# Kernel tuning notes

Hardware: AMD Instinct MI355X
Metric: run time of the kernel (lower is better)

Reference implementation:

```python
import jax, jax.numpy as jnp
import numpy as np

F = 128   # num_features
H = 128   # hidden sizes
U = 128   # u_size == out_size
N = 50000
E = 600000
B = 64
L = 4     # hops + 1 layers


def _scatter_mean(vals, idx, num_segments):
    s = jax.ops.segment_sum(vals, idx, num_segments=num_segments)
    cnt = jax.ops.segment_sum(jnp.ones((vals.shape[0],), vals.dtype), idx,
                              num_segments=num_segments)
    return s / jnp.maximum(cnt, 1.0)[:, None]


def setup_inputs() -> dict:
    key = jax.random.key(0)
    ks = jax.random.split(key, 20)
    x = jax.random.normal(ks[0], (N, F), jnp.float32)
    edge_index = jax.random.randint(ks[1], (2, E), 0, N, jnp.int64)
    u = jax.random.normal(ks[2], (B, U), jnp.float32)
    batch = jnp.sort(jax.random.randint(ks[3], (N,), 0, B, jnp.int64))
    sc = 0.05
    # stacked per-layer params (all layer dims identical since u_size==out_size)
    params = {
        'n1w1': jax.random.normal(ks[4], (L, F, H), jnp.float32) * sc,
        'n1b1': jnp.zeros((L, H), jnp.float32),
        'n1w2': jax.random.normal(ks[5], (L, H, H), jnp.float32) * sc,
        'n1b2': jnp.zeros((L, H), jnp.float32),
        'n2w1': jax.random.normal(ks[6], (L, F + H + U, H), jnp.float32) * sc,
        'n2b1': jnp.zeros((L, H), jnp.float32),
        'n2w2': jax.random.normal(ks[7], (L, H, F), jnp.float32) * sc,
        'n2b2': jnp.zeros((L, F), jnp.float32),
        'gw1': jax.random.normal(ks[8], (L, F + U, H), jnp.float32) * sc,
        'gb1': jnp.zeros((L, H), jnp.float32),
        'gw2': jax.random.normal(ks[9], (L, H, U), jnp.float32) * sc,
        'gb2': jnp.zeros((L, U), jnp.float32),
    }
    return dict(x=x, edge_index=edge_index, u=u, batch=batch, **params)


def reference(x, edge_index, u, batch,
              n1w1, n1b1, n1w2, n1b2, n2w1, n2b1, n2w2, n2b2,
              gw1, gb1, gw2, gb2):
    row, col = edge_index[0], edge_index[1]
    for l in range(L):
        # NodeModel
        m = jax.nn.relu(x[row] @ n1w1[l] + n1b1[l]) @ n1w2[l] + n1b2[l]  # [E,H]
        agg = _scatter_mean(m, col, N)                                    # [N,H]
        h = jnp.concatenate([x, agg, u[batch]], axis=1)                   # [N,F+H+U]
        x = jax.nn.relu(h @ n2w1[l] + n2b1[l]) @ n2w2[l] + n2b2[l]        # [N,F]
        # GlobalModel (uses updated x)
        g = jnp.concatenate([u, _scatter_mean(x, batch, B)], axis=1)      # [B,F+U]
        u = jax.nn.relu(g @ gw1[l] + gb1[l]) @ gw2[l] + gb2[l]            # [B,U]
    return (x, u)
```

## Files before the change

kernel.cpp:

```cpp
#include <hip/hip_runtime.h>

typedef __bf16 bf16;
typedef bf16 bf16x8 __attribute__((ext_vector_type(8)));
typedef bf16 bf16x4 __attribute__((ext_vector_type(4)));
typedef bf16 bf16x2 __attribute__((ext_vector_type(2)));
typedef float floatx4 __attribute__((ext_vector_type(4)));

#define MFMA __builtin_amdgcn_mfma_f32_16x16x32_bf16

__device__ __forceinline__ float bfhi_f(unsigned u) {
  const unsigned x = u << 16;
  return __builtin_bit_cast(float, x);
}
__device__ __forceinline__ float bflo_f(unsigned u) {
  const unsigned x = u & 0xffff0000u;
  return __builtin_bit_cast(float, x);
}

__device__ __forceinline__ void bar_lds() {
  asm volatile("s_waitcnt lgkmcnt(0)" ::: "memory");
  __builtin_amdgcn_s_barrier();
}


__global__ void hist_kernel(const int* __restrict__ ei, int* __restrict__ cnt, int E) {
  int e = blockIdx.x * blockDim.x + threadIdx.x;
  if (e < E) atomicAdd(&cnt[ei[E + e]], 1);
}

__global__ void gcnt_kernel(const int* __restrict__ batch, int* __restrict__ gcnt,
                            int N, int B) {
  const int b = threadIdx.x;
  if (b >= B) return;
  auto lb = [&](int v) {
    int lo = 0, hi = N;
    while (lo < hi) {
      const int mid = (lo + hi) >> 1;
      if (batch[mid] < v) lo = mid + 1; else hi = mid;
    }
    return lo;
  };
  gcnt[b] = lb(b + 1) - lb(b);
}

__global__ void scan1_kernel(const int* __restrict__ cnt, int* __restrict__ colptr,
                             int* __restrict__ rctr, int* __restrict__ btot, int n) {
  __shared__ int sd[256];
  const int tid = threadIdx.x;
  const int i0 = blockIdx.x * 2048 + tid * 8;
  int v[8];
  int tot = 0;
#pragma unroll
  for (int j = 0; j < 8; ++j) {
    const int i = i0 + j;
    v[j] = (i < n) ? cnt[i] : 0;
    tot += v[j];
  }
  sd[tid] = tot;
  __syncthreads();
  for (int off = 1; off < 256; off <<= 1) {
    const int t = (tid >= off) ? sd[tid - off] : 0;
    __syncthreads();
    sd[tid] += t;
    __syncthreads();
  }
  int excl = sd[tid] - tot;
#pragma unroll
  for (int j = 0; j < 8; ++j) {
    const int i = i0 + j;
    if (i < n) { colptr[i] = excl; rctr[i] = excl; }
    excl += v[j];
  }
  if (tid == 255) btot[blockIdx.x] = sd[255];
}

__global__ void scan2_kernel(int* __restrict__ colptr, int* __restrict__ rctr,
                             const int* __restrict__ btot, int n) {
  __shared__ int off_s;
  const int tid = threadIdx.x;
  if (blockIdx.x == 0) return;
  if (tid == 0) {
    int o = 0;
    for (int j = 0; j < (int)blockIdx.x; ++j) o += btot[j];
    off_s = o;
  }
  __syncthreads();
  const int off = off_s;
  const int i0 = blockIdx.x * 2048 + tid * 8;
#pragma unroll
  for (int j = 0; j < 8; ++j) {
    const int i = i0 + j;
    if (i < n) { colptr[i] += off; rctr[i] += off; }
  }
}

__global__ void place_kernel(const int* __restrict__ ei, int* __restrict__ rctr,
                             int* __restrict__ esrow, int E) {
  int e = blockIdx.x * blockDim.x + threadIdx.x;
  if (e >= E) return;
  const int r = ei[e];
  const int c = ei[E + e];
  const int p = atomicAdd(&rctr[c], 1);
  esrow[p] = r;
}

__global__ void wsplit_kernel(const float* __restrict__ src, bf16* __restrict__ dst,
                              int Ksrc, int K, int HH) {
  const int l = blockIdx.y;
  const int gid = blockIdx.x * blockDim.x + threadIdx.x;
  if (gid >= K * HH) return;
  const int h = gid / K, k = gid - h * K;
  const float v = src[(size_t)l * Ksrc * HH + (size_t)k * HH + h];
  const bf16 hi = (bf16)v;
  const bf16 lo = (bf16)(v - (float)hi);
  bf16* d = dst + (size_t)l * 2 * K * HH;
  d[(size_t)h * K + k] = hi;
  d[(size_t)K * HH + (size_t)h * K + k] = lo;
}

__global__ void wfuse_kernel(const float* __restrict__ n2w1,
                             const float* __restrict__ n1w2,
                             float* __restrict__ G) {
  const int l = blockIdx.y, k = blockIdx.x, h = threadIdx.x;
  const float* w = n2w1 + (size_t)l * 384 * 128;
  float* g = G + (size_t)l * 256 * 128;
  g[(size_t)k * 128 + h] = w[(size_t)k * 128 + h];
  const float* a = n1w2 + (size_t)l * 128 * 128 + (size_t)k * 128;
  float s = 0.f;
#pragma unroll 8
  for (int j = 0; j < 128; ++j)
    s = fmaf(a[j], w[(size_t)(128 + j) * 128 + h], s);
  g[(size_t)(128 + k) * 128 + h] = s;
}

__global__ void xsplit_kernel(const float* __restrict__ x, bf16* __restrict__ xhi,
                              bf16* __restrict__ xlo, int n4) {
  const int i = blockIdx.x * 256 + threadIdx.x;
  if (i >= n4) return;
  const float4 v = ((const float4*)x)[i];
  bf16x4 h, l;
  const float vv[4] = {v.x, v.y, v.z, v.w};
#pragma unroll
  for (int r = 0; r < 4; ++r) {
    h[r] = (bf16)vv[r];
    l[r] = (bf16)(vv[r] - (float)h[r]);
  }
  *(bf16x4*)&xhi[(size_t)i * 4] = h;
  *(bf16x4*)&xlo[(size_t)i * 4] = l;
}

__global__ __launch_bounds__(256, 3)
void pnode_mfma(const bf16* __restrict__ xh, const bf16* __restrict__ xl,
                const bf16* __restrict__ w1t, const float* __restrict__ b1,
                bf16* __restrict__ P, int N) {
  __shared__ __align__(16) bf16 R[64 * 136];

  const int tid = threadIdx.x;
  const int n0 = blockIdx.x * 64;
  const int wave = tid >> 6, lane = tid & 63, q = lane >> 4, lr = lane & 15;
  const int hbase = wave * 32;

  int nn[4];
#pragma unroll
  for (int nt = 0; nt < 4; ++nt) {
    int n = n0 + nt * 16 + lr;
    nn[nt] = (n > N - 1) ? (N - 1) : n;
  }

  const floatx4 zz = {0.f, 0.f, 0.f, 0.f};
  floatx4 acc[2][4];
#pragma unroll
  for (int mt = 0; mt < 2; ++mt)
#pragma unroll
    for (int nt = 0; nt < 4; ++nt) acc[mt][nt] = zz;

  {
    bf16x8 bh[2][4], bl[2][4], ah[2][2], al[2][2];
    auto loadA = [&](int kc, int buf) {
#pragma unroll
      for (int mt = 0; mt < 2; ++mt) {
        const bf16* wp = w1t + (size_t)(hbase + mt * 16 + lr) * 128 + kc * 32 + q * 8;
        ah[buf][mt] = *(const bf16x8*)wp;
        al[buf][mt] = *(const bf16x8*)(wp + 16384);
      }
    };
    auto loadB = [&](int kc, int buf) {
#pragma unroll
      for (int nt = 0; nt < 4; ++nt) {
        const size_t off = (size_t)nn[nt] * 128 + kc * 32 + q * 8;
        bh[buf][nt] = *(const bf16x8*)(xh + off);
        bl[buf][nt] = *(const bf16x8*)(xl + off);
      }
    };
    loadA(0, 0);
    loadB(0, 0);
#pragma unroll
    for (int kc = 0; kc < 4; ++kc) {
      const int cur = kc & 1, nxt = cur ^ 1;
      if (kc < 3) {
        loadA(kc + 1, nxt);
        loadB(kc + 1, nxt);
      }
#pragma unroll
      for (int nt = 0; nt < 4; ++nt)
#pragma unroll
        for (int mt = 0; mt < 2; ++mt) {
          acc[mt][nt] = MFMA(ah[cur][mt], bh[cur][nt], acc[mt][nt], 0, 0, 0);
          acc[mt][nt] = MFMA(al[cur][mt], bh[cur][nt], acc[mt][nt], 0, 0, 0);
          acc[mt][nt] = MFMA(ah[cur][mt], bl[cur][nt], acc[mt][nt], 0, 0, 0);
        }
    }
  }

#pragma unroll
  for (int mt = 0; mt < 2; ++mt) {
    const int h0 = hbase + mt * 16 + q * 4;
    const float* bp = &b1[h0];
#pragma unroll
    for (int nt = 0; nt < 4; ++nt) {
      const int e = nt * 16 + lr;
      bf16x4 hh;
#pragma unroll
      for (int r = 0; r < 4; ++r)
        hh[r] = (bf16)fmaxf(acc[mt][nt][r] + bp[r], 0.f);
      *(bf16x4*)&R[e * 136 + h0] = hh;
    }
  }
  bar_lds();
#pragma unroll
  for (int it = 0; it < 4; ++it) {
    const int idx = it * 256 + tid;
    const int row = idx >> 4;
    const int f8 = (idx & 15) * 8;
    const int n = n0 + row;
    if (n < N)
      *(bf16x8*)&P[(size_t)n * 128 + f8] = *(const bf16x8*)&R[row * 136 + f8];
  }
}

__global__ __launch_bounds__(256, 8)
void agg_csr(const bf16* __restrict__ P, const int* __restrict__ colptr,
             const int* __restrict__ esrow,
             bf16* __restrict__ aggh, bf16* __restrict__ aggl, int N, int E) {
  const int lane = threadIdx.x & 63;
  const int c = blockIdx.x * 4 + (threadIdx.x >> 6);
  if (c >= N) return;
  const int beg = colptr[c];
  const int end = (c == N - 1) ? E : colptr[c + 1];
  float s0[4] = {0.f, 0.f, 0.f, 0.f};
  float s1[4] = {0.f, 0.f, 0.f, 0.f};
  int e = beg;
  for (; e + 8 <= end; e += 8) {
    int r[8];
#pragma unroll
    for (int j = 0; j < 8; ++j) r[j] = esrow[e + j];
    unsigned v[8];
#pragma unroll
    for (int j = 0; j < 8; ++j)
      v[j] = *(const unsigned*)&P[(size_t)r[j] * 128 + lane * 2];
#pragma unroll
    for (int j = 0; j < 8; ++j) {
      s0[j & 3] += bfhi_f(v[j]);
      s1[j & 3] += bflo_f(v[j]);
    }
  }
  const int rem = end - e;
  if (rem > 0) {
    int r[8];
#pragma unroll
    for (int j = 0; j < 8; ++j) r[j] = esrow[e + (j < rem ? j : 0)];
    unsigned v[8];
#pragma unroll
    for (int j = 0; j < 8; ++j)
      v[j] = *(const unsigned*)&P[(size_t)r[j] * 128 + lane * 2];
#pragma unroll
    for (int j = 0; j < 8; ++j) {
      if (j < rem) {
        s0[j & 3] += bfhi_f(v[j]);
        s1[j & 3] += bflo_f(v[j]);
      }
    }
  }
  const int cc = end - beg;
  const float inv = 1.f / (float)(cc > 1 ? cc : 1);
  const float v0 = ((s0[0] + s0[1]) + (s0[2] + s0[3])) * inv;
  const float v1 = ((s1[0] + s1[1]) + (s1[2] + s1[3])) * inv;
  bf16x2 h, l;
  h[0] = (bf16)v0;  l[0] = (bf16)(v0 - (float)h[0]);
  h[1] = (bf16)v1;  l[1] = (bf16)(v1 - (float)h[1]);
  *(bf16x2*)&aggh[(size_t)c * 128 + lane * 2] = h;
  *(bf16x2*)&aggl[(size_t)c * 128 + lane * 2] = l;
}

__global__ __launch_bounds__(256, 3)
void node_p(bf16* xh, bf16* xl,
            const bf16* __restrict__ aggh, const bf16* __restrict__ aggl,
            const float* __restrict__ UW, const int* __restrict__ batch,
            const bf16* __restrict__ w1t, const bf16* __restrict__ w2t,
            const float* __restrict__ b2,
            const bf16* __restrict__ w1te, const float* __restrict__ b1e,
            bf16* __restrict__ Pout, float* __restrict__ gx,
            float* __restrict__ xout, int write_x, int has_next, int N) {
  __shared__ __align__(16) bf16 R[2 * 64 * 136];
  __shared__ int sbatch[64];

  const int tid = threadIdx.x;
  const int n0 = blockIdx.x * 64;
  const int wave = tid >> 6, lane = tid & 63, q = lane >> 4, lr = lane & 15;
  const int hbase = wave * 32;

  if (tid < 64) {
    int n = n0 + tid;
    sbatch[tid] = batch[(n > N - 1) ? (N - 1) : n];
  }

  int nn[4], ub[4];
#pragma unroll
  for (int nt = 0; nt < 4; ++nt) {
    int n = n0 + nt * 16 + lr;
    if (n > N - 1) n = N - 1;
    nn[nt] = n;
    ub[nt] = batch[n];
  }

  floatx4 acc[2][4];
#pragma unroll
  for (int mt = 0; mt < 2; ++mt)
#pragma unroll
    for (int nt = 0; nt < 4; ++nt)
      acc[mt][nt] = *(const floatx4*)&UW[(size_t)ub[nt] * 128 + hbase + mt * 16 + q * 4];

  {
    bf16x8 bh[2][4], bl[2][4], ah[2][2], al[2][2];
    auto loadB = [&](int kc, int buf) {
#pragma unroll
      for (int nt = 0; nt < 4; ++nt) {
        if (kc < 4) {
          const size_t off = (size_t)nn[nt] * 128 + kc * 32 + q * 8;
          bh[buf][nt] = *(const bf16x8*)(xh + off);
          bl[buf][nt] = *(const bf16x8*)(xl + off);
        } else {
          const size_t off = (size_t)nn[nt] * 128 + (kc - 4) * 32 + q * 8;
          bh[buf][nt] = *(const bf16x8*)(aggh + off);
          bl[buf][nt] = *(const bf16x8*)(aggl + off);
        }
      }
    };
    auto loadA = [&](int kc, int buf) {
#pragma unroll
      for (int mt = 0; mt < 2; ++mt) {
        const bf16* wp = w1t + (size_t)(hbase + mt * 16 + lr) * 256 + kc * 32 + q * 8;
        ah[buf][mt] = *(const bf16x8*)wp;
        al[buf][mt] = *(const bf16x8*)(wp + 32768);
      }
    };
    loadA(0, 0);
    loadB(0, 0);
#pragma unroll
    for (int kc = 0; kc < 8; ++kc) {
      const int cur = kc & 1, nxt = cur ^ 1;
      if (kc < 7) {
        loadA(kc + 1, nxt);
        loadB(kc + 1, nxt);
      }
#pragma unroll
      for (int nt = 0; nt < 4; ++nt)
#pragma unroll
        for (int mt = 0; mt < 2; ++mt) {
          acc[mt][nt] = MFMA(ah[cur][mt], bh[cur][nt], acc[mt][nt], 0, 0, 0);
          acc[mt][nt] = MFMA(al[cur][mt], bh[cur][nt], acc[mt][nt], 0, 0, 0);
          acc[mt][nt] = MFMA(ah[cur][mt], bl[cur][nt], acc[mt][nt], 0, 0, 0);
        }
    }
  }

  bf16x8 a2h[2][2], a2l[2][2];
#pragma unroll
  for (int mt = 0; mt < 2; ++mt) {
    const bf16* wp = w2t + (size_t)(hbase + mt * 16 + lr) * 128 + q * 8;
    a2h[0][mt] = *(const bf16x8*)wp;
    a2l[0][mt] = *(const bf16x8*)(wp + 16384);
  }

  const floatx4 zz = {0.f, 0.f, 0.f, 0.f};
#pragma unroll
  for (int mt = 0; mt < 2; ++mt) {
    const int h0 = hbase + mt * 16 + q * 4;
#pragma unroll
    for (int nt = 0; nt < 4; ++nt) {
      const int e = nt * 16 + lr;
      bf16x4 hh, ll;
#pragma unroll
      for (int r = 0; r < 4; ++r) {
        const float v = fmaxf(acc[mt][nt][r], 0.f);
        hh[r] = (bf16)v;
        ll[r] = (bf16)(v - (float)hh[r]);
      }
      *(bf16x4*)&R[e * 136 + h0] = hh;
      *(bf16x4*)&R[64 * 136 + e * 136 + h0] = ll;
      acc[mt][nt] = zz;
    }
  }
  bar_lds();

#pragma unroll
  for (int ks = 0; ks < 4; ++ks) {
    const int cur = ks & 1, nxt = cur ^ 1;
    if (ks < 3) {
#pragma unroll
      for (int mt = 0; mt < 2; ++mt) {
        const bf16* wp = w2t + (size_t)(hbase + mt * 16 + lr) * 128 + (ks + 1) * 32 + q * 8;
        a2h[nxt][mt] = *(const bf16x8*)wp;
        a2l[nxt][mt] = *(const bf16x8*)(wp + 16384);
      }
    }
    bf16x8 b2h[4], b2l[4];
#pragma unroll
    for (int nt = 0; nt < 4; ++nt) {
      const bf16* hp = &R[(nt * 16 + lr) * 136 + ks * 32 + q * 8];
      b2h[nt] = *(const bf16x8*)hp;
      b2l[nt] = *(const bf16x8*)(hp + 64 * 136);
    }
#pragma unroll
    for (int nt = 0; nt < 4; ++nt)
#pragma unroll
      for (int mt = 0; mt < 2; ++mt) {
        acc[mt][nt] = MFMA(a2h[cur][mt], b2h[nt], acc[mt][nt], 0, 0, 0);
        acc[mt][nt] = MFMA(a2l[cur][mt], b2h[nt], acc[mt][nt], 0, 0, 0);
        acc[mt][nt] = MFMA(a2h[cur][mt], b2l[nt], acc[mt][nt], 0, 0, 0);
      }
  }
  bar_lds();

  bf16x8 pah[2][2], pal[2][2];
  if (has_next) {
#pragma unroll
    for (int mt = 0; mt < 2; ++mt) {
      const bf16* wp = w1te + (size_t)(hbase + mt * 16 + lr) * 128 + q * 8;
      pah[0][mt] = *(const bf16x8*)wp;
      pal[0][mt] = *(const bf16x8*)(wp + 16384);
    }
  }

  float* Xt = (float*)&R[0];
#pragma unroll
  for (int mt = 0; mt < 2; ++mt) {
    const int f0 = hbase + mt * 16 + q * 4;
    const float* bp = &b2[f0];
#pragma unroll
    for (int nt = 0; nt < 4; ++nt) {
      const int e = nt * 16 + lr;
      const int n = n0 + e;
      float4 o;
      o.x = (n < N) ? acc[mt][nt][0] + bp[0] : 0.f;
      o.y = (n < N) ? acc[mt][nt][1] + bp[1] : 0.f;
      o.z = (n < N) ? acc[mt][nt][2] + bp[2] : 0.f;
      o.w = (n < N) ? acc[mt][nt][3] + bp[3] : 0.f;
      *(float4*)&Xt[e * 132 + f0] = o;
    }
  }
  bar_lds();

  if (has_next) {
#pragma unroll
    for (int it = 0; it < 4; ++it) {
      const int idx = it * 256 + tid;
      const int row = idx >> 4;
      const int f8 = (idx & 15) * 8;
      const int n = n0 + row;
      if (n < N) {
        bf16x8 hh, ll;
#pragma unroll
        for (int j = 0; j < 8; ++j) {
          const float v = Xt[row * 132 + f8 + j];
          hh[j] = (bf16)v;
          ll[j] = (bf16)(v - (float)hh[j]);
        }
        *(bf16x8*)&xh[(size_t)n * 128 + f8] = hh;
        *(bf16x8*)&xl[(size_t)n * 128 + f8] = ll;
      }
    }
  }
  if (write_x) {
#pragma unroll
    for (int it = 0; it < 8; ++it) {
      const int idx = it * 256 + tid;
      const int row = idx >> 5;
      const int f4 = (idx & 31) * 4;
      const int n = n0 + row;
      if (n < N)
        *(float4*)&xout[(size_t)n * 128 + f4] = *(const float4*)&Xt[row * 132 + f4];
    }
  }

  {
    const int f = tid & 127;
    const int es = (tid >> 7) * 32;
    int cur = sbatch[es];
    float s = 0.f;
    for (int e = es; e < es + 32; ++e) {
      const int b = sbatch[e];
      const float v = Xt[e * 132 + f];
      if (b != cur) {
        atomicAdd(&gx[(size_t)cur * 128 + f], s);
        s = 0.f;
        cur = b;
      }
      s += v;
    }
    atomicAdd(&gx[(size_t)cur * 128 + f], s);
  }

  if (!has_next) return;

  floatx4 pacc[2][4];
#pragma unroll
  for (int mt = 0; mt < 2; ++mt)
#pragma unroll
    for (int nt = 0; nt < 4; ++nt) pacc[mt][nt] = zz;

#pragma unroll
  for (int kc = 0; kc < 4; ++kc) {
    const int cur = kc & 1, nxt = cur ^ 1;
    if (kc < 3) {
#pragma unroll
      for (int mt = 0; mt < 2; ++mt) {
        const bf16* wp = w1te + (size_t)(hbase + mt * 16 + lr) * 128 + (kc + 1) * 32 + q * 8;
        pah[nxt][mt] = *(const bf16x8*)wp;
        pal[nxt][mt] = *(const bf16x8*)(wp + 16384);
      }
    }
    bf16x8 bh[4], bl[4];
#pragma unroll
    for (int nt = 0; nt < 4; ++nt) {
      const float* xp = &Xt[(nt * 16 + lr) * 132 + kc * 32 + q * 8];
#pragma unroll
      for (int r = 0; r < 8; ++r) {
        const float v = xp[r];
        bh[nt][r] = (bf16)v;
        bl[nt][r] = (bf16)(v - (float)bh[nt][r]);
      }
    }
#pragma unroll
    for (int nt = 0; nt < 4; ++nt)
#pragma unroll
      for (int mt = 0; mt < 2; ++mt) {
        pacc[mt][nt] = MFMA(pah[cur][mt], bh[nt], pacc[mt][nt], 0, 0, 0);
        pacc[mt][nt] = MFMA(pal[cur][mt], bh[nt], pacc[mt][nt], 0, 0, 0);
        pacc[mt][nt] = MFMA(pah[cur][mt], bl[nt], pacc[mt][nt], 0, 0, 0);
      }
  }
  bar_lds();

#pragma unroll
  for (int mt = 0; mt < 2; ++mt) {
    const int h0 = hbase + mt * 16 + q * 4;
    const float* bp = &b1e[h0];
#pragma unroll
    for (int nt = 0; nt < 4; ++nt) {
      const int e = nt * 16 + lr;
      bf16x4 hh;
#pragma unroll
      for (int r = 0; r < 4; ++r)
        hh[r] = (bf16)fmaxf(pacc[mt][nt][r] + bp[r], 0.f);
      *(bf16x4*)&R[e * 136 + h0] = hh;
    }
  }
  bar_lds();
#pragma unroll
  for (int it = 0; it < 4; ++it) {
    const int idx = it * 256 + tid;
    const int row = idx >> 4;
    const int f8 = (idx & 15) * 8;
    const int n = n0 + row;
    if (n < N)
      *(bf16x8*)&Pout[(size_t)n * 128 + f8] = *(const bf16x8*)&R[row * 136 + f8];
  }
}

__global__ void uw_kernel(const float* __restrict__ u, const float* __restrict__ w1,
                          const float* __restrict__ b1, const float* __restrict__ pb,
                          float* __restrict__ UW) {
  const int b = blockIdx.x, h = threadIdx.x;
  float s = b1[h];
#pragma unroll 8
  for (int k = 0; k < 128; ++k)
    s = fmaf(u[b * 128 + k], w1[(size_t)(256 + k) * 128 + h], s);
#pragma unroll 8
  for (int k = 0; k < 128; ++k)
    s = fmaf(pb[k], w1[(size_t)(128 + k) * 128 + h], s);
  UW[b * 128 + h] = s;
}

__global__ __launch_bounds__(128)
void gmlp_kernel(const float* __restrict__ uin, float* __restrict__ gx,
                 const int* __restrict__ gcnt,
                 const float* __restrict__ gw1, const float* __restrict__ gb1,
                 const float* __restrict__ gw2, const float* __restrict__ gb2,
                 float* __restrict__ uout,
                 const float* __restrict__ w1n_next,
                 const float* __restrict__ b1n_next,
                 const float* __restrict__ pb_next,
                 float* __restrict__ UW, int has_next) {
  __shared__ float g[256];
  __shared__ float g1[128];
  const int b = blockIdx.x;
  const int t = threadIdx.x;
  const int c = gcnt[b];
  const float inv = 1.f / (float)(c > 1 ? c : 1);
  g[t] = uin[b * 128 + t];
  g[128 + t] = gx[b * 128 + t] * inv;
  gx[b * 128 + t] = 0.f;
  __syncthreads();
  float acc = gb1[t];
#pragma unroll 8
  for (int k = 0; k < 256; ++k) acc = fmaf(g[k], gw1[k * 128 + t], acc);
  g1[t] = fmaxf(acc, 0.f);
  __syncthreads();
  float acc2 = gb2[t];
#pragma unroll 8
  for (int k = 0; k < 128; ++k) acc2 = fmaf(g1[k], gw2[k * 128 + t], acc2);
  uout[b * 128 + t] = acc2;
  if (has_next) {
    __syncthreads();
    g[t] = acc2;
    __syncthreads();
    float s = b1n_next[t];
#pragma unroll 8
    for (int k = 0; k < 128; ++k)
      s = fmaf(g[k], w1n_next[(size_t)(256 + k) * 128 + t], s);
#pragma unroll 8
    for (int k = 0; k < 128; ++k)
      s = fmaf(pb_next[k], w1n_next[(size_t)(128 + k) * 128 + t], s);
    UW[b * 128 + t] = s;
  }
}

extern "C" void kernel_launch(void* const* d_in, const int* in_sizes, int n_in,
                              void* d_out, int out_size, void* d_ws, size_t ws_size,
                              hipStream_t stream) {
  constexpr int N = 50000, E = 600000, B = 64, F = 128, L = 4;

  const float* x0    = (const float*)d_in[0];
  const int*   ei    = (const int*)  d_in[1];
  const float* u0    = (const float*)d_in[2];
  const int*   batch = (const int*)  d_in[3];
  const float* n1w1  = (const float*)d_in[4];
  const float* n1b1  = (const float*)d_in[5];
  const float* n1w2  = (const float*)d_in[6];
  const float* n1b2  = (const float*)d_in[7];
  const float* n2w1  = (const float*)d_in[8];
  const float* n2b1  = (const float*)d_in[9];
  const float* n2w2  = (const float*)d_in[10];
  const float* n2b2  = (const float*)d_in[11];
  const float* gw1   = (const float*)d_in[12];
  const float* gb1   = (const float*)d_in[13];
  const float* gw2   = (const float*)d_in[14];
  const float* gb2   = (const float*)d_in[15];
  float* out = (float*)d_out;

  char* p = (char*)d_ws;
  auto carve = [&](size_t bytes) -> void* {
    void* q = (void*)p;
    p += (bytes + 255) & ~(size_t)255;
    return q;
  };
  float* ubuf  = (float*)carve((size_t)B * F * 4);
  float* gx    = (float*)carve((size_t)B * F * 4);
  float* UW    = (float*)carve((size_t)B * F * 4);
  int*   cnt   = (int*)carve((size_t)N * 4);
  int*   colptr= (int*)carve((size_t)(N + 1) * 4);
  int*   rctr  = (int*)carve((size_t)N * 4);
  int*   gcnt  = (int*)carve((size_t)B * 4);
  int*   btot  = (int*)carve(32 * 4);
  int*   esrow = (int*)carve((size_t)E * 4);
  bf16*  xhi   = (bf16*)carve((size_t)N * F * 2);
  bf16*  xlo   = (bf16*)carve((size_t)N * F * 2);
  bf16*  P_a   = (bf16*)carve((size_t)N * F * 2);
  bf16*  P_b   = (bf16*)carve((size_t)N * F * 2);
  bf16*  aggh  = (bf16*)carve((size_t)N * F * 2);
  bf16*  aggl  = (bf16*)carve((size_t)N * F * 2);
  bf16*  w1t_e = (bf16*)carve((size_t)L * 2 * 128 * 128 * 2);
  bf16*  w1t_n = (bf16*)carve((size_t)L * 2 * 256 * 128 * 2);
  bf16*  w2t_n = (bf16*)carve((size_t)L * 2 * 128 * 128 * 2);
  float* wtmp  = (float*)carve((size_t)L * 256 * 128 * 4);

  constexpr int SCAN_BLOCKS = (N + 2047) / 2048;

  hipMemsetAsync(cnt, 0, (size_t)N * 4, stream);
  hipMemsetAsync(gx, 0, (size_t)B * F * 4, stream);
  hist_kernel<<<(E + 255) / 256, 256, 0, stream>>>(ei, cnt, E);
  gcnt_kernel<<<1, 64, 0, stream>>>(batch, gcnt, N, B);
  scan1_kernel<<<SCAN_BLOCKS, 256, 0, stream>>>(cnt, colptr, rctr, btot, N);
  scan2_kernel<<<SCAN_BLOCKS, 256, 0, stream>>>(colptr, rctr, btot, N);
  place_kernel<<<(E + 255) / 256, 256, 0, stream>>>(ei, rctr, esrow, E);
  wsplit_kernel<<<dim3(64, L), 256, 0, stream>>>(n1w1, w1t_e, 128, 128, 128);
  wfuse_kernel<<<dim3(128, L), 128, 0, stream>>>(n2w1, n1w2, wtmp);
  wsplit_kernel<<<dim3(128, L), 256, 0, stream>>>(wtmp, w1t_n, 256, 256, 128);
  wsplit_kernel<<<dim3(64, L), 256, 0, stream>>>(n2w2, w2t_n, 128, 128, 128);
  xsplit_kernel<<<(N * F / 4 + 255) / 256, 256, 0, stream>>>(x0, xhi, xlo, N * F / 4);
  uw_kernel<<<B, 128, 0, stream>>>(u0, n2w1, n2b1, n1b2, UW);

  const int NB = (N + 63) / 64;
  pnode_mfma<<<NB, 256, 0, stream>>>(xhi, xlo, w1t_e, n1b1, P_a, N);

  for (int l = 0; l < L; ++l) {
    const float* uin  = l ? ubuf : u0;
    float*       uout = (l == L - 1) ? out + (size_t)N * F : ubuf;
    const int    wx   = (l == L - 1) ? 1 : 0;
    const int    hn   = (l < L - 1) ? 1 : 0;
    const bf16*  Pin  = (l & 1) ? P_b : P_a;
    bf16*        Pout = (l & 1) ? P_a : P_b;
    const int    le   = hn ? (l + 1) : l;

    agg_csr<<<(N + 3) / 4, 256, 0, stream>>>(Pin, colptr, esrow, aggh, aggl, N, E);
    node_p<<<NB, 256, 0, stream>>>(
        xhi, xlo, aggh, aggl, UW, batch,
        w1t_n + (size_t)l * 65536, w2t_n + (size_t)l * 32768,
        n2b2 + l * 128,
        w1t_e + (size_t)le * 32768, n1b1 + le * 128,
        Pout, gx, out, wx, hn, N);
    gmlp_kernel<<<B, 128, 0, stream>>>(
        uin, gx, gcnt,
        gw1 + (size_t)l * 256 * 128, gb1 + l * 128,
        gw2 + (size_t)l * 128 * 128, gb2 + l * 128, uout,
        hn ? (n2w1 + (size_t)(l + 1) * 384 * 128) : n2w1,
        hn ? (n2b1 + (l + 1) * 128) : n2b1,
        hn ? (n1b2 + (l + 1) * 128) : n1b2,
        UW, hn);
  }
}
```

Baseline: 695.7 us.

## Fuse global MLP into aggregation launch and widen node kernel to 512 threads

The per-layer global MLP is moved into extra blocks appended to the agg_csr grid, so the graph-level update for layer l runs alongside the edge aggregation for layer l+1. This removes a separate small kernel launch and its serialization per layer. The node kernel also goes from 256 to 512 threads, each wave covering 16 hidden rows instead of 32. That halves per-wave accumulator registers and raises the number of waves per block. In exchange, agg_csr carries extra shared memory and parameters, and there is more barrier traffic per node block.

```diff
diff --git a/kernel.cpp b/kernel.cpp
--- a/kernel.cpp
+++ b/kernel.cpp
@@ -238,10 +238,74 @@
   }
 }
 
+__device__ __forceinline__ void gmlp_dev(
+    int b, int t, const float* __restrict__ uin, float* __restrict__ gx,
+    const int* __restrict__ gcnt,
+    const float* __restrict__ gw1, const float* __restrict__ gb1,
+    const float* __restrict__ gw2, const float* __restrict__ gb2,
+    float* __restrict__ uout,
+    const float* __restrict__ w1n, const float* __restrict__ b1n,
+    const float* __restrict__ pbn, float* __restrict__ UW, int has_next) {
+  __shared__ float g[256];
+  __shared__ float g1[128];
+  const bool act = t < 128;
+  const int c = gcnt[b];
+  const float inv = 1.f / (float)(c > 1 ? c : 1);
+  if (act) {
+    g[t] = uin[b * 128 + t];
+    g[128 + t] = gx[b * 128 + t] * inv;
+    gx[b * 128 + t] = 0.f;
+  }
+  __syncthreads();
+  float acc = 0.f;
+  if (act) {
+    acc = gb1[t];
+#pragma unroll 8
+    for (int k = 0; k < 256; ++k) acc = fmaf(g[k], gw1[k * 128 + t], acc);
+    g1[t] = fmaxf(acc, 0.f);
+  }
+  __syncthreads();
+  float acc2 = 0.f;
+  if (act) {
+    acc2 = gb2[t];
+#pragma unroll 8
+    for (int k = 0; k < 128; ++k) acc2 = fmaf(g1[k], gw2[k * 128 + t], acc2);
+    uout[b * 128 + t] = acc2;
+  }
+  if (has_next) {
+    __syncthreads();
+    if (act) g[t] = acc2;
+    __syncthreads();
+    if (act) {
+      float s = b1n[t];
+#pragma unroll 8
+      for (int k = 0; k < 128; ++k)
+        s = fmaf(g[k], w1n[(size_t)(256 + k) * 128 + t], s);
+#pragma unroll 8
+      for (int k = 0; k < 128; ++k)
+        s = fmaf(pbn[k], w1n[(size_t)(128 + k) * 128 + t], s);
+      UW[b * 128 + t] = s;
+    }
+  }
+}
+
 __global__ __launch_bounds__(256, 8)
 void agg_csr(const bf16* __restrict__ P, const int* __restrict__ colptr,
              const int* __restrict__ esrow,
-             bf16* __restrict__ aggh, bf16* __restrict__ aggl, int N, int E) {
+             bf16* __restrict__ aggh, bf16* __restrict__ aggl, int N, int E,
+             int nAgg,
+             const float* __restrict__ uin, float* __restrict__ gx,
+             const int* __restrict__ gcnt,
+             const float* __restrict__ gw1, const float* __restrict__ gb1,
+             const float* __restrict__ gw2, const float* __restrict__ gb2,
+             float* __restrict__ uout,
+             const float* __restrict__ w1n, const float* __restrict__ b1n,
+             const float* __restrict__ pbn, float* __restrict__ UW) {
+  if ((int)blockIdx.x >= nAgg) {
+    gmlp_dev(blockIdx.x - nAgg, threadIdx.x, uin, gx, gcnt, gw1, gb1, gw2, gb2,
+             uout, w1n, b1n, pbn, UW, 1);
+    return;
+  }
   const int lane = threadIdx.x & 63;
   const int c = blockIdx.x * 4 + (threadIdx.x >> 6);
   if (c >= N) return;
@@ -292,7 +356,7 @@
   *(bf16x2*)&aggl[(size_t)c * 128 + lane * 2] = l;
 }
 
-__global__ __launch_bounds__(256, 3)
+__global__ __launch_bounds__(512, 4)
 void node_p(bf16* xh, bf16* xl,
             const bf16* __restrict__ aggh, const bf16* __restrict__ aggl,
             const float* __restrict__ UW, const int* __restrict__ batch,
@@ -307,7 +371,7 @@
   const int tid = threadIdx.x;
   const int n0 = blockIdx.x * 64;
   const int wave = tid >> 6, lane = tid & 63, q = lane >> 4, lr = lane & 15;
-  const int hbase = wave * 32;
+  const int hbase = wave * 16;
 
   if (tid < 64) {
     int n = n0 + tid;
@@ -323,15 +387,13 @@
     ub[nt] = batch[n];
   }
 
-  floatx4 acc[2][4];
-#pragma unroll
-  for (int mt = 0; mt < 2; ++mt)
-#pragma unroll
-    for (int nt = 0; nt < 4; ++nt)
-      acc[mt][nt] = *(const floatx4*)&UW[(size_t)ub[nt] * 128 + hbase + mt * 16 + q * 4];
+  floatx4 acc[4];
+#pragma unroll
+  for (int nt = 0; nt < 4; ++nt)
+    acc[nt] = *(const floatx4*)&UW[(size_t)ub[nt] * 128 + hbase + q * 4];
 
   {
-    bf16x8 bh[2][4], bl[2][4], ah[2][2], al[2][2];
+    bf16x8 bh[2][4], bl[2][4], ah[2], al[2];
     auto loadB = [&](int kc, int buf) {
 #pragma unroll
       for (int nt = 0; nt < 4; ++nt) {
@@ -347,12 +409,9 @@
       }
     };
     auto loadA = [&](int kc, int buf) {
-#pragma unroll
-      for (int mt = 0; mt < 2; ++mt) {
-        const bf16* wp = w1t + (size_t)(hbase + mt * 16 + lr) * 256 + kc * 32 + q * 8;
-        ah[buf][mt] = *(const bf16x8*)wp;
-        al[buf][mt] = *(const bf16x8*)(wp + 32768);
-      }
+      const bf16* wp = w1t + (size_t)(hbase + lr) * 256 + kc * 32 + q * 8;
+      ah[buf] = *(const bf16x8*)wp;
+      al[buf] = *(const bf16x8*)(wp + 32768);
     };
     loadA(0, 0);
     loadB(0, 0);
@@ -364,42 +423,36 @@
         loadB(kc + 1, nxt);
       }
 #pragma unroll
-      for (int nt = 0; nt < 4; ++nt)
-#pragma unroll
-        for (int mt = 0; mt < 2; ++mt) {
-          acc[mt][nt] = MFMA(ah[cur][mt], bh[cur][nt], acc[mt][nt], 0, 0, 0);
-          acc[mt][nt] = MFMA(al[cur][mt], bh[cur][nt], acc[mt][nt], 0, 0, 0);
-          acc[mt][nt] = MFMA(ah[cur][mt], bl[cur][nt], acc[mt][nt], 0, 0, 0);
-        }
-    }
-  }
-
-  bf16x8 a2h[2][2], a2l[2][2];
-#pragma unroll
-  for (int mt = 0; mt < 2; ++mt) {
-    const bf16* wp = w2t + (size_t)(hbase + mt * 16 + lr) * 128 + q * 8;
-    a2h[0][mt] = *(const bf16x8*)wp;
-    a2l[0][mt] = *(const bf16x8*)(wp + 16384);
+      for (int nt = 0; nt < 4; ++nt) {
+        acc[nt] = MFMA(ah[cur], bh[cur][nt], acc[nt], 0, 0, 0);
+        acc[nt] = MFMA(al[cur], bh[cur][nt], acc[nt], 0, 0, 0);
+        acc[nt] = MFMA(ah[cur], bl[cur][nt], acc[nt], 0, 0, 0);
+      }
+    }
+  }
+
+  bf16x8 a2h[2], a2l[2];
+  {
+    const bf16* wp = w2t + (size_t)(hbase + lr) * 128 + q * 8;
+    a2h[0] = *(const bf16x8*)wp;
+    a2l[0] = *(const bf16x8*)(wp + 16384);
   }
 
   const floatx4 zz = {0.f, 0.f, 0.f, 0.f};
-#pragma unroll
-  for (int mt = 0; mt < 2; ++mt) {
-    const int h0 = hbase + mt * 16 + q * 4;
-#pragma unroll
-    for (int nt = 0; nt < 4; ++nt) {
-      const int e = nt * 16 + lr;
-      bf16x4 hh, ll;
-#pragma unroll
-      for (int r = 0; r < 4; ++r) {
-        const float v = fmaxf(acc[mt][nt][r], 0.f);
-        hh[r] = (bf16)v;
-        ll[r] = (bf16)(v - (float)hh[r]);
-      }
-      *(bf16x4*)&R[e * 136 + h0] = hh;
-      *(bf16x4*)&R[64 * 136 + e * 136 + h0] = ll;
-      acc[mt][nt] = zz;
-    }
+  const int h0 = hbase + q * 4;
+#pragma unroll
+  for (int nt = 0; nt < 4; ++nt) {
+    const int e = nt * 16 + lr;
+    bf16x4 hh, ll;
+#pragma unroll
+    for (int r = 0; r < 4; ++r) {
+      const float v = fmaxf(acc[nt][r], 0.f);
+      hh[r] = (bf16)v;
+      ll[r] = (bf16)(v - (float)hh[r]);
+    }
+    *(bf16x4*)&R[e * 136 + h0] = hh;
+    *(bf16x4*)&R[64 * 136 + e * 136 + h0] = ll;
+    acc[nt] = zz;
   }
   bar_lds();
 
@@ -407,12 +460,9 @@
   for (int ks = 0; ks < 4; ++ks) {
     const int cur = ks & 1, nxt = cur ^ 1;
     if (ks < 3) {
-#pragma unroll
-      for (int mt = 0; mt < 2; ++mt) {
-        const bf16* wp = w2t + (size_t)(hbase + mt * 16 + lr) * 128 + (ks + 1) * 32 + q * 8;
-        a2h[nxt][mt] = *(const bf16x8*)wp;
-        a2l[nxt][mt] = *(const bf16x8*)(wp + 16384);
-      }
+      const bf16* wp = w2t + (size_t)(hbase + lr) * 128 + (ks + 1) * 32 + q * 8;
+      a2h[nxt] = *(const bf16x8*)wp;
+      a2l[nxt] = *(const bf16x8*)(wp + 16384);
     }
     bf16x8 b2h[4], b2l[4];
 #pragma unroll
@@ -422,49 +472,42 @@
       b2l[nt] = *(const bf16x8*)(hp + 64 * 136);
     }
 #pragma unroll
-    for (int nt = 0; nt < 4; ++nt)
-#pragma unroll
-      for (int mt = 0; mt < 2; ++mt) {
-        acc[mt][nt] = MFMA(a2h[cur][mt], b2h[nt], acc[mt][nt], 0, 0, 0);
-        acc[mt][nt] = MFMA(a2l[cur][mt], b2h[nt], acc[mt][nt], 0, 0, 0);
-        acc[mt][nt] = MFMA(a2h[cur][mt], b2l[nt], acc[mt][nt], 0, 0, 0);
-      }
+    for (int nt = 0; nt < 4; ++nt) {
+      acc[nt] = MFMA(a2h[cur], b2h[nt], acc[nt], 0, 0, 0);
+      acc[nt] = MFMA(a2l[cur], b2h[nt], acc[nt], 0, 0, 0);
+      acc[nt] = MFMA(a2h[cur], b2l[nt], acc[nt], 0, 0, 0);
+    }
   }
   bar_lds();
 
-  bf16x8 pah[2][2], pal[2][2];
+  bf16x8 pah[2], pal[2];
   if (has_next) {
-#pragma unroll
-    for (int mt = 0; mt < 2; ++mt) {
-      const bf16* wp = w1te + (size_t)(hbase + mt * 16 + lr) * 128 + q * 8;
-      pah[0][mt] = *(const bf16x8*)wp;
-      pal[0][mt] = *(const bf16x8*)(wp + 16384);
-    }
+    const bf16* wp = w1te + (size_t)(hbase + lr) * 128 + q * 8;
+    pah[0] = *(const bf16x8*)wp;
+    pal[0] = *(const bf16x8*)(wp + 16384);
   }
 
   float* Xt = (float*)&R[0];
-#pragma unroll
-  for (int mt = 0; mt < 2; ++mt) {
-    const int f0 = hbase + mt * 16 + q * 4;
-    const float* bp = &b2[f0];
+  {
+    const float* bp = &b2[h0];
 #pragma unroll
     for (int nt = 0; nt < 4; ++nt) {
       const int e = nt * 16 + lr;
       const int n = n0 + e;
       float4 o;
-      o.x = (n < N) ? acc[mt][nt][0] + bp[0] : 0.f;
-      o.y = (n < N) ? acc[mt][nt][1] + bp[1] : 0.f;
-      o.z = (n < N) ? acc[mt][nt][2] + bp[2] : 0.f;
-      o.w = (n < N) ? acc[mt][nt][3] + bp[3] : 0.f;
-      *(float4*)&Xt[e * 132 + f0] = o;
+      o.x = (n < N) ? acc[nt][0] + bp[0] : 0.f;
+      o.y = (n < N) ? acc[nt][1] + bp[1] : 0.f;
+      o.z = (n < N) ? acc[nt][2] + bp[2] : 0.f;
+      o.w = (n < N) ? acc[nt][3] + bp[3] : 0.f;
+      *(float4*)&Xt[e * 132 + h0] = o;
     }
   }
   bar_lds();
 
   if (has_next) {
 #pragma unroll
-    for (int it = 0; it < 4; ++it) {
-      const int idx = it * 256 + tid;
+    for (int it = 0; it < 2; ++it) {
+      const int idx = it * 512 + tid;
       const int row = idx >> 4;
       const int f8 = (idx & 15) * 8;
       const int n = n0 + row;
@@ -483,8 +526,8 @@
   }
   if (write_x) {
 #pragma unroll
-    for (int it = 0; it < 8; ++it) {
-      const int idx = it * 256 + tid;
+    for (int it = 0; it < 4; ++it) {
+      const int idx = it * 512 + tid;
       const int row = idx >> 5;
       const int f4 = (idx & 31) * 4;
       const int n = n0 + row;
@@ -495,10 +538,10 @@
 
   {
     const int f = tid & 127;
-    const int es = (tid >> 7) * 32;
+    const int es = (tid >> 7) * 16;
     int cur = sbatch[es];
     float s = 0.f;
-    for (int e = es; e < es + 32; ++e) {
+    for (int e = es; e < es + 16; ++e) {
       const int b = sbatch[e];
       const float v = Xt[e * 132 + f];
       if (b != cur) {
@@ -513,22 +556,17 @@
 
   if (!has_next) return;
 
-  floatx4 pacc[2][4];
-#pragma unroll
-  for (int mt = 0; mt < 2; ++mt)
-#pragma unroll
-    for (int nt = 0; nt < 4; ++nt) pacc[mt][nt] = zz;
+  floatx4 pacc[4];
+#pragma unroll
+  for (int nt = 0; nt < 4; ++nt) pacc[nt] = zz;
 
 #pragma unroll
   for (int kc = 0; kc < 4; ++kc) {
     const int cur = kc & 1, nxt = cur ^ 1;
     if (kc < 3) {
-#pragma unroll
-      for (int mt = 0; mt < 2; ++mt) {
-        const bf16* wp = w1te + (size_t)(hbase + mt * 16 + lr) * 128 + (kc + 1) * 32 + q * 8;
-        pah[nxt][mt] = *(const bf16x8*)wp;
-        pal[nxt][mt] = *(const bf16x8*)(wp + 16384);
-      }
+      const bf16* wp = w1te + (size_t)(hbase + lr) * 128 + (kc + 1) * 32 + q * 8;
+      pah[nxt] = *(const bf16x8*)wp;
+      pal[nxt] = *(const bf16x8*)(wp + 16384);
     }
     bf16x8 bh[4], bl[4];
 #pragma unroll
@@ -542,19 +580,15 @@
       }
     }
 #pragma unroll
-    for (int nt = 0; nt < 4; ++nt)
-#pragma unroll
-      for (int mt = 0; mt < 2; ++mt) {
-        pacc[mt][nt] = MFMA(pah[cur][mt], bh[nt], pacc[mt][nt], 0, 0, 0);
-        pacc[mt][nt] = MFMA(pal[cur][mt], bh[nt], pacc[mt][nt], 0, 0, 0);
-        pacc[mt][nt] = MFMA(pah[cur][mt], bl[nt], pacc[mt][nt], 0, 0, 0);
-      }
+    for (int nt = 0; nt < 4; ++nt) {
+      pacc[nt] = MFMA(pah[cur], bh[nt], pacc[nt], 0, 0, 0);
+      pacc[nt] = MFMA(pal[cur], bh[nt], pacc[nt], 0, 0, 0);
+      pacc[nt] = MFMA(pah[cur], bl[nt], pacc[nt], 0, 0, 0);
+    }
   }
   bar_lds();
 
-#pragma unroll
-  for (int mt = 0; mt < 2; ++mt) {
-    const int h0 = hbase + mt * 16 + q * 4;
+  {
     const float* bp = &b1e[h0];
 #pragma unroll
     for (int nt = 0; nt < 4; ++nt) {
@@ -562,14 +596,14 @@
       bf16x4 hh;
 #pragma unroll
       for (int r = 0; r < 4; ++r)
-        hh[r] = (bf16)fmaxf(pacc[mt][nt][r] + bp[r], 0.f);
+        hh[r] = (bf16)fmaxf(pacc[nt][r] + bp[r], 0.f);
       *(bf16x4*)&R[e * 136 + h0] = hh;
     }
   }
   bar_lds();
 #pragma unroll
-  for (int it = 0; it < 4; ++it) {
-    const int idx = it * 256 + tid;
+  for (int it = 0; it < 2; ++it) {
+    const int idx = it * 512 + tid;
     const int row = idx >> 4;
     const int f8 = (idx & 15) * 8;
     const int n = n0 + row;
@@ -598,42 +632,11 @@
                  const float* __restrict__ gw1, const float* __restrict__ gb1,
                  const float* __restrict__ gw2, const float* __restrict__ gb2,
                  float* __restrict__ uout,
-                 const float* __restrict__ w1n_next,
-                 const float* __restrict__ b1n_next,
-                 const float* __restrict__ pb_next,
-                 float* __restrict__ UW, int has_next) {
-  __shared__ float g[256];
-  __shared__ float g1[128];
-  const int b = blockIdx.x;
-  const int t = threadIdx.x;
-  const int c = gcnt[b];
-  const float inv = 1.f / (float)(c > 1 ? c : 1);
-  g[t] = uin[b * 128 + t];
-  g[128 + t] = gx[b * 128 + t] * inv;
-  gx[b * 128 + t] = 0.f;
-  __syncthreads();
-  float acc = gb1[t];
-#pragma unroll 8
-  for (int k = 0; k < 256; ++k) acc = fmaf(g[k], gw1[k * 128 + t], acc);
-  g1[t] = fmaxf(acc, 0.f);
-  __syncthreads();
-  float acc2 = gb2[t];
-#pragma unroll 8
-  for (int k = 0; k < 128; ++k) acc2 = fmaf(g1[k], gw2[k * 128 + t], acc2);
-  uout[b * 128 + t] = acc2;
-  if (has_next) {
-    __syncthreads();
-    g[t] = acc2;
-    __syncthreads();
-    float s = b1n_next[t];
-#pragma unroll 8
-    for (int k = 0; k < 128; ++k)
-      s = fmaf(g[k], w1n_next[(size_t)(256 + k) * 128 + t], s);
-#pragma unroll 8
-    for (int k = 0; k < 128; ++k)
-      s = fmaf(pb_next[k], w1n_next[(size_t)(128 + k) * 128 + t], s);
-    UW[b * 128 + t] = s;
-  }
+                 const float* __restrict__ w1n, const float* __restrict__ b1n,
+                 const float* __restrict__ pbn, float* __restrict__ UW,
+                 int has_next) {
+  gmlp_dev(blockIdx.x, threadIdx.x, uin, gx, gcnt, gw1, gb1, gw2, gb2,
+           uout, w1n, b1n, pbn, UW, has_next);
 }
 
 extern "C" void kernel_launch(void* const* d_in, const int* in_sizes, int n_in,
@@ -702,31 +705,41 @@
   uw_kernel<<<B, 128, 0, stream>>>(u0, n2w1, n2b1, n1b2, UW);
 
   const int NB = (N + 63) / 64;
+  const int NAGG = (N + 3) / 4;
   pnode_mfma<<<NB, 256, 0, stream>>>(xhi, xlo, w1t_e, n1b1, P_a, N);
 
+  agg_csr<<<NAGG, 256, 0, stream>>>(P_a, colptr, esrow, aggh, aggl, N, E, NAGG,
+      u0, gx, gcnt, gw1, gb1, gw2, gb2, ubuf, n2w1, n2b1, n1b2, UW);
+
   for (int l = 0; l < L; ++l) {
-    const float* uin  = l ? ubuf : u0;
-    float*       uout = (l == L - 1) ? out + (size_t)N * F : ubuf;
     const int    wx   = (l == L - 1) ? 1 : 0;
     const int    hn   = (l < L - 1) ? 1 : 0;
-    const bf16*  Pin  = (l & 1) ? P_b : P_a;
     bf16*        Pout = (l & 1) ? P_a : P_b;
     const int    le   = hn ? (l + 1) : l;
 
-    agg_csr<<<(N + 3) / 4, 256, 0, stream>>>(Pin, colptr, esrow, aggh, aggl, N, E);
-    node_p<<<NB, 256, 0, stream>>>(
+    node_p<<<NB, 512, 0, stream>>>(
         xhi, xlo, aggh, aggl, UW, batch,
         w1t_n + (size_t)l * 65536, w2t_n + (size_t)l * 32768,
         n2b2 + l * 128,
         w1t_e + (size_t)le * 32768, n1b1 + le * 128,
         Pout, gx, out, wx, hn, N);
-    gmlp_kernel<<<B, 128, 0, stream>>>(
-        uin, gx, gcnt,
-        gw1 + (size_t)l * 256 * 128, gb1 + l * 128,
-        gw2 + (size_t)l * 128 * 128, gb2 + l * 128, uout,
-        hn ? (n2w1 + (size_t)(l + 1) * 384 * 128) : n2w1,
-        hn ? (n2b1 + (l + 1) * 128) : n2b1,
-        hn ? (n1b2 + (l + 1) * 128) : n1b2,
-        UW, hn);
-  }
-}
+
+    if (l < L - 1) {
+      agg_csr<<<NAGG + B, 256, 0, stream>>>(
+          Pout, colptr, esrow, aggh, aggl, N, E, NAGG,
+          (l ? ubuf : u0), gx, gcnt,
+          gw1 + (size_t)l * 256 * 128, gb1 + l * 128,
+          gw2 + (size_t)l * 128 * 128, gb2 + l * 128,
+          ubuf,
+          n2w1 + (size_t)(l + 1) * 384 * 128, n2b1 + (l + 1) * 128,
+          n1b2 + (l + 1) * 128, UW);
+    } else {
+      gmlp_kernel<<<B, 128, 0, stream>>>(
+          ubuf, gx, gcnt,
+          gw1 + (size_t)l * 256 * 128, gb1 + l * 128,
+          gw2 + (size_t)l * 128 * 128, gb2 + l * 128,
+          out + (size_t)N * F,
+          n2w1, n2b1, n1b2, UW, 0);
+    }
+  }
+}
```

Measured after the change: 793.4 us. +14.0%, slower.

## Fuse global MLP into aggregation launch and widen per-lane edge gathers

Applied to the files above, without the earlier changes.

The global-model MLP blocks are appended as extra blocks to the next layer's CSR aggregation kernel, so three separate gmlp launches go away and the small per-graph MLP runs alongside the aggregation. The aggregation itself now has each half-wave handle a different edge with 8-byte loads of four bf16 features, and the two halves are combined with a cross-lane shuffle. This halves the number of gather load instructions per edge for the same bytes in flight. The cost is heavier agg blocks, shared memory declared for the gmlp path, and the gmlp blocks competing with aggregation blocks for the same compute units.

```diff
diff --git a/kernel.cpp b/kernel.cpp
--- a/kernel.cpp
+++ b/kernel.cpp
@@ -238,58 +238,138 @@
   }
 }
 
+__device__ __forceinline__ void gmlp_dev(
+    int b, int t, const float* __restrict__ uin, float* __restrict__ gx,
+    const int* __restrict__ gcnt,
+    const float* __restrict__ gw1, const float* __restrict__ gb1,
+    const float* __restrict__ gw2, const float* __restrict__ gb2,
+    float* __restrict__ uout,
+    const float* __restrict__ w1n, const float* __restrict__ b1n,
+    const float* __restrict__ pbn, float* __restrict__ UW, int has_next) {
+  __shared__ float g[256];
+  __shared__ float g1[128];
+  const bool act = t < 128;
+  const int c = gcnt[b];
+  const float inv = 1.f / (float)(c > 1 ? c : 1);
+  if (act) {
+    g[t] = uin[b * 128 + t];
+    g[128 + t] = gx[b * 128 + t] * inv;
+    gx[b * 128 + t] = 0.f;
+  }
+  __syncthreads();
+  float acc = 0.f;
+  if (act) {
+    acc = gb1[t];
+#pragma unroll 8
+    for (int k = 0; k < 256; ++k) acc = fmaf(g[k], gw1[k * 128 + t], acc);
+    g1[t] = fmaxf(acc, 0.f);
+  }
+  __syncthreads();
+  float acc2 = 0.f;
+  if (act) {
+    acc2 = gb2[t];
+#pragma unroll 8
+    for (int k = 0; k < 128; ++k) acc2 = fmaf(g1[k], gw2[k * 128 + t], acc2);
+    uout[b * 128 + t] = acc2;
+  }
+  if (has_next) {
+    __syncthreads();
+    if (act) g[t] = acc2;
+    __syncthreads();
+    if (act) {
+      float s = b1n[t];
+#pragma unroll 8
+      for (int k = 0; k < 128; ++k)
+        s = fmaf(g[k], w1n[(size_t)(256 + k) * 128 + t], s);
+#pragma unroll 8
+      for (int k = 0; k < 128; ++k)
+        s = fmaf(pbn[k], w1n[(size_t)(128 + k) * 128 + t], s);
+      UW[b * 128 + t] = s;
+    }
+  }
+}
+
 __global__ __launch_bounds__(256, 8)
 void agg_csr(const bf16* __restrict__ P, const int* __restrict__ colptr,
              const int* __restrict__ esrow,
-             bf16* __restrict__ aggh, bf16* __restrict__ aggl, int N, int E) {
+             bf16* __restrict__ aggh, bf16* __restrict__ aggl, int N, int E,
+             int nAgg,
+             const float* __restrict__ uin, float* __restrict__ gx,
+             const int* __restrict__ gcnt,
+             const float* __restrict__ gw1, const float* __restrict__ gb1,
+             const float* __restrict__ gw2, const float* __restrict__ gb2,
+             float* __restrict__ uout,
+             const float* __restrict__ w1n, const float* __restrict__ b1n,
+             const float* __restrict__ pbn, float* __restrict__ UW) {
+  if ((int)blockIdx.x >= nAgg) {
+    gmlp_dev(blockIdx.x - nAgg, threadIdx.x, uin, gx, gcnt, gw1, gb1, gw2, gb2,
+             uout, w1n, b1n, pbn, UW, 1);
+    return;
+  }
   const int lane = threadIdx.x & 63;
   const int c = blockIdx.x * 4 + (threadIdx.x >> 6);
   if (c >= N) return;
+  const int p = lane >> 5;
+  const int fl = lane & 31;
   const int beg = colptr[c];
   const int end = (c == N - 1) ? E : colptr[c + 1];
-  float s0[4] = {0.f, 0.f, 0.f, 0.f};
-  float s1[4] = {0.f, 0.f, 0.f, 0.f};
+  float s[4] = {0.f, 0.f, 0.f, 0.f};
   int e = beg;
   for (; e + 8 <= end; e += 8) {
-    int r[8];
-#pragma unroll
-    for (int j = 0; j < 8; ++j) r[j] = esrow[e + j];
-    unsigned v[8];
-#pragma unroll
-    for (int j = 0; j < 8; ++j)
-      v[j] = *(const unsigned*)&P[(size_t)r[j] * 128 + lane * 2];
-#pragma unroll
-    for (int j = 0; j < 8; ++j) {
-      s0[j & 3] += bfhi_f(v[j]);
-      s1[j & 3] += bflo_f(v[j]);
+    int r[4];
+#pragma unroll
+    for (int j = 0; j < 4; ++j) r[j] = esrow[e + 2 * j + p];
+    uint2 v[4];
+#pragma unroll
+    for (int j = 0; j < 4; ++j)
+      v[j] = *(const uint2*)&P[(size_t)r[j] * 128 + fl * 4];
+#pragma unroll
+    for (int j = 0; j < 4; ++j) {
+      s[0] += bfhi_f(v[j].x);
+      s[1] += bflo_f(v[j].x);
+      s[2] += bfhi_f(v[j].y);
+      s[3] += bflo_f(v[j].y);
     }
   }
   const int rem = end - e;
   if (rem > 0) {
-    int r[8];
-#pragma unroll
-    for (int j = 0; j < 8; ++j) r[j] = esrow[e + (j < rem ? j : 0)];
-    unsigned v[8];
-#pragma unroll
-    for (int j = 0; j < 8; ++j)
-      v[j] = *(const unsigned*)&P[(size_t)r[j] * 128 + lane * 2];
-#pragma unroll
-    for (int j = 0; j < 8; ++j) {
-      if (j < rem) {
-        s0[j & 3] += bfhi_f(v[j]);
-        s1[j & 3] += bflo_f(v[j]);
-      }
-    }
-  }
+    int r[4];
+    bool m[4];
+#pragma unroll
+    for (int j = 0; j < 4; ++j) {
+      const int idx = 2 * j + p;
+      m[j] = idx < rem;
+      r[j] = esrow[e + (m[j] ? idx : 0)];
+    }
+    uint2 v[4];
+#pragma unroll
+    for (int j = 0; j < 4; ++j)
+      v[j] = *(const uint2*)&P[(size_t)r[j] * 128 + fl * 4];
+#pragma unroll
+    for (int j = 0; j < 4; ++j) {
+      if (m[j]) {
+        s[0] += bfhi_f(v[j].x);
+        s[1] += bflo_f(v[j].x);
+        s[2] += bfhi_f(v[j].y);
+        s[3] += bflo_f(v[j].y);
+      }
+    }
+  }
+#pragma unroll
+  for (int k = 0; k < 4; ++k) s[k] += __shfl_xor(s[k], 32);
   const int cc = end - beg;
   const float inv = 1.f / (float)(cc > 1 ? cc : 1);
-  const float v0 = ((s0[0] + s0[1]) + (s0[2] + s0[3])) * inv;
-  const float v1 = ((s1[0] + s1[1]) + (s1[2] + s1[3])) * inv;
-  bf16x2 h, l;
-  h[0] = (bf16)v0;  l[0] = (bf16)(v0 - (float)h[0]);
-  h[1] = (bf16)v1;  l[1] = (bf16)(v1 - (float)h[1]);
-  *(bf16x2*)&aggh[(size_t)c * 128 + lane * 2] = h;
-  *(bf16x2*)&aggl[(size_t)c * 128 + lane * 2] = l;
+  if (p == 0) {
+    bf16x4 h4, l4;
+#pragma unroll
+    for (int k = 0; k < 4; ++k) {
+      const float v = s[k] * inv;
+      h4[k] = (bf16)v;
+      l4[k] = (bf16)(v - (float)h4[k]);
+    }
+    *(bf16x4*)&aggh[(size_t)c * 128 + fl * 4] = h4;
+    *(bf16x4*)&aggl[(size_t)c * 128 + fl * 4] = l4;
+  }
 }
 
 __global__ __launch_bounds__(256, 3)
@@ -598,42 +678,11 @@
                  const float* __restrict__ gw1, const float* __restrict__ gb1,
                  const float* __restrict__ gw2, const float* __restrict__ gb2,
                  float* __restrict__ uout,
-                 const float* __restrict__ w1n_next,
-                 const float* __restrict__ b1n_next,
-                 const float* __restrict__ pb_next,
-                 float* __restrict__ UW, int has_next) {
-  __shared__ float g[256];
-  __shared__ float g1[128];
-  const int b = blockIdx.x;
-  const int t = threadIdx.x;
-  const int c = gcnt[b];
-  const float inv = 1.f / (float)(c > 1 ? c : 1);
-  g[t] = uin[b * 128 + t];
-  g[128 + t] = gx[b * 128 + t] * inv;
-  gx[b * 128 + t] = 0.f;
-  __syncthreads();
-  float acc = gb1[t];
-#pragma unroll 8
-  for (int k = 0; k < 256; ++k) acc = fmaf(g[k], gw1[k * 128 + t], acc);
-  g1[t] = fmaxf(acc, 0.f);
-  __syncthreads();
-  float acc2 = gb2[t];
-#pragma unroll 8
-  for (int k = 0; k < 128; ++k) acc2 = fmaf(g1[k], gw2[k * 128 + t], acc2);
-  uout[b * 128 + t] = acc2;
-  if (has_next) {
-    __syncthreads();
-    g[t] = acc2;
-    __syncthreads();
-    float s = b1n_next[t];
-#pragma unroll 8
-    for (int k = 0; k < 128; ++k)
-      s = fmaf(g[k], w1n_next[(size_t)(256 + k) * 128 + t], s);
-#pragma unroll 8
-    for (int k = 0; k < 128; ++k)
-      s = fmaf(pb_next[k], w1n_next[(size_t)(128 + k) * 128 + t], s);
-    UW[b * 128 + t] = s;
-  }
+                 const float* __restrict__ w1n, const float* __restrict__ b1n,
+                 const float* __restrict__ pbn, float* __restrict__ UW,
+                 int has_next) {
+  gmlp_dev(blockIdx.x, threadIdx.x, uin, gx, gcnt, gw1, gb1, gw2, gb2,
+           uout, w1n, b1n, pbn, UW, has_next);
 }
 
 extern "C" void kernel_launch(void* const* d_in, const int* in_sizes, int n_in,
@@ -702,31 +751,41 @@
   uw_kernel<<<B, 128, 0, stream>>>(u0, n2w1, n2b1, n1b2, UW);
 
   const int NB = (N + 63) / 64;
+  const int NAGG = (N + 3) / 4;
   pnode_mfma<<<NB, 256, 0, stream>>>(xhi, xlo, w1t_e, n1b1, P_a, N);
 
+  agg_csr<<<NAGG, 256, 0, stream>>>(P_a, colptr, esrow, aggh, aggl, N, E, NAGG,
+      u0, gx, gcnt, gw1, gb1, gw2, gb2, ubuf, n2w1, n2b1, n1b2, UW);
+
   for (int l = 0; l < L; ++l) {
-    const float* uin  = l ? ubuf : u0;
-    float*       uout = (l == L - 1) ? out + (size_t)N * F : ubuf;
     const int    wx   = (l == L - 1) ? 1 : 0;
     const int    hn   = (l < L - 1) ? 1 : 0;
-    const bf16*  Pin  = (l & 1) ? P_b : P_a;
     bf16*        Pout = (l & 1) ? P_a : P_b;
     const int    le   = hn ? (l + 1) : l;
 
-    agg_csr<<<(N + 3) / 4, 256, 0, stream>>>(Pin, colptr, esrow, aggh, aggl, N, E);
     node_p<<<NB, 256, 0, stream>>>(
         xhi, xlo, aggh, aggl, UW, batch,
         w1t_n + (size_t)l * 65536, w2t_n + (size_t)l * 32768,
         n2b2 + l * 128,
         w1t_e + (size_t)le * 32768, n1b1 + le * 128,
         Pout, gx, out, wx, hn, N);
-    gmlp_kernel<<<B, 128, 0, stream>>>(
-        uin, gx, gcnt,
-        gw1 + (size_t)l * 256 * 128, gb1 + l * 128,
-        gw2 + (size_t)l * 128 * 128, gb2 + l * 128, uout,
-        hn ? (n2w1 + (size_t)(l + 1) * 384 * 128) : n2w1,
-        hn ? (n2b1 + (l + 1) * 128) : n2b1,
-        hn ? (n1b2 + (l + 1) * 128) : n1b2,
-        UW, hn);
-  }
-}
+
+    if (l < L - 1) {
+      agg_csr<<<NAGG + B, 256, 0, stream>>>(
+          Pout, colptr, esrow, aggh, aggl, N, E, NAGG,
+          (l ? ubuf : u0), gx, gcnt,
+          gw1 + (size_t)l * 256 * 128, gb1 + l * 128,
+          gw2 + (size_t)l * 128 * 128, gb2 + l * 128,
+          ubuf,
+          n2w1 + (size_t)(l + 1) * 384 * 128, n2b1 + (l + 1) * 128,
+          n1b2 + (l + 1) * 128, UW);
+    } else {
+      gmlp_kernel<<<B, 128, 0, stream>>>(
+          ubuf, gx, gcnt,
+          gw1 + (size_t)l * 256 * 128, gb1 + l * 128,
+          gw2 + (size_t)l * 128 * 128, gb2 + l * 128,
+          out + (size_t)N * F,
+          n2w1, n2b1, n1b2, UW, 0);
+    }
+  }
+}
```

New measurement: 701.5 us. No clear change (+0.8%).
